# Optimization experiments

Measured on AMD Instinct MI355X. Metric: run time of the kernel, lower is better.

Reference implementation:

```python
import jax, jax.numpy as jnp
import numpy as np

N_ITERS = 10
OMEGA = 10
W_HALF = 512          # hpm.W
D = 2 * W_HALF        # real-lifted signal dim
BATCH = 4096
P_PREV = 8
EPS = 1e-8


def hard_thr(x, omega=OMEGA):
    # x: [B, D]; keep the omega largest-|x| entries per row, zero the rest
    # (equivalent to torch scatter-zero of the D-omega smallest |x|)
    _, idx = jax.lax.top_k(jnp.abs(x), omega)            # [B, omega]
    rows = jnp.arange(x.shape[0])[:, None]
    mask = jnp.zeros_like(x).at[rows, idx].set(1.0)
    return x * mask


def _spectral_density(z):
    # z: [B, D] -> squared complex magnitude summed over batch, min-max normalized
    w = z.shape[1] // 2
    p = z[:, :w] ** 2 + z[:, w:] ** 2                    # [B, W] (sign flip of imag part cancels)
    mD = p.sum(0)                                        # [W]
    return (mD - mD.min()) / (mD.max() - mD.min() + EPS)


def setup_inputs() -> dict:
    key = jax.random.key(0)
    k0, k1, k2 = jax.random.split(key, 3)
    x = jax.random.normal(k0, (BATCH, D), jnp.float32)
    prev_windows = jax.random.normal(k1, (P_PREV, BATCH, D), jnp.float32)
    # learned dictionary (stand-in for the real-lifted partial Fourier matrix)
    W_d = jax.random.normal(k2, (1, D, D), jnp.float32) / np.sqrt(D).astype(np.float32)
    L = jnp.float32(5.0)                                 # hpm.L (fixed Lipschitz constant)
    S = jnp.eye(D, dtype=jnp.float32)[None] - (1.0 / L) * jnp.matmul(
        jnp.swapaxes(W_d, 1, 2), W_d)                    # [1, D, D]
    lambda2 = jnp.float32(1.0)
    return {"x": x, "prev_windows": prev_windows, "W_d": W_d, "S": S,
            "lambda2": lambda2, "L": L}


def reference(x, prev_windows, W_d, S, lambda2, L):
    Wd0 = W_d[0]                                         # [D, D]
    S0 = S[0]                                            # [D, D]
    w = D // 2

    # B = (1/L * W_d) @ x   (column-vector matvec as row GEMM)
    b = (x @ Wd0.T) / L                                  # [B, D]

    # two warm-up ISTA/IHT steps
    z = hard_thr(b)
    c = b + z @ S0.T
    z = hard_thr(c)

    mD_normalized = _spectral_density(z)                 # [W]

    # ---- attention over previous windows (prev_windows non-empty branch) ----
    pw = prev_windows                                    # [P, B, D]
    p_prev = pw[:, :, :w] ** 2 + pw[:, :, w:] ** 2       # [P, B, W]
    mD_prev = p_prev.sum(1)                              # [P, W]
    mn = mD_prev.min(axis=1, keepdims=True)
    mx = mD_prev.max(axis=1, keepdims=True)
    prev_mDn = (mD_prev - mn) / (mx - mn + EPS)          # [P, W]

    att = prev_mDn @ mD_normalized[:, None]              # [P, 1]
    att = jax.nn.softmax(att / np.sqrt(float(w)).astype(np.float32), axis=0)
    pw_clamped = jnp.clip(pw, -150.0, 150.0)
    z = (pw_clamped * att[:, None]).sum(0) * lambda2     # [B, D]

    # ---- unrolled iterations ----
    for _ in range(N_ITERS):
        c = b + z @ S0.T
        z = hard_thr(c)

    mD_normalized = _spectral_density(z)                 # [W]
    return (mD_normalized, z)
```

## Files before the change

### kernel.cpp

```cpp
#include <hip/hip_runtime.h>
#include <stdint.h>

#define BATCH 4096
#define DIM   1024
#define PPREV 8

__device__ __forceinline__ int wave_max_i32(int v) {
    #pragma unroll
    for (int m = 1; m < 64; m <<= 1) v = max(v, __shfl_xor(v, m));
    return v;
}
__device__ __forceinline__ int wave_min_i32(int v) {
    #pragma unroll
    for (int m = 1; m < 64; m <<= 1) v = min(v, __shfl_xor(v, m));
    return v;
}
__device__ __forceinline__ int wave_sum_i32(int v) {
    #pragma unroll
    for (int m = 1; m < 64; m <<= 1) v += __shfl_xor(v, m);
    return v;
}
__device__ __forceinline__ int wave_exscan_i32(int v, int lane) {
    int s = v;
    #pragma unroll
    for (int off = 1; off < 64; off <<= 1) {
        int o = __shfl_up(s, off);
        s += (lane >= off) ? o : 0;
    }
    return s - v;
}


__device__ __forceinline__ int bound10_tbits(const int k[16], int lane) {
    int lm = k[0];
    #pragma unroll
    for (int s = 1; s < 16; ++s) lm = max(lm, k[s]);
    int cur = lm, tb = 0;
    #pragma unroll
    for (int r = 0; r < 10; ++r) {
        int m = wave_max_i32(cur);
        tb = m;
        unsigned long long ball = __ballot(cur == m);
        int wl = (int)__ffsll(ball) - 1;
        if (lane == wl) cur = 0;
    }
    return tb;
}

__device__ __forceinline__ void top10_full(const int kin[16], int sgn, int lane,
                                           int wi[10], float wv[10]) {
    int k[16];
    #pragma unroll
    for (int s = 0; s < 16; ++s) k[s] = kin[s];
    #pragma unroll
    for (int r = 0; r < 10; ++r) {
        int lm = k[0]; int ls = 0;
        #pragma unroll
        for (int s = 1; s < 16; ++s) { if (k[s] > lm) { lm = k[s]; ls = s; } }
        int m = wave_max_i32(lm);
        int cj = (lm == m) ? ((lane << 4) | ls) : 4096;
        int jw = wave_min_i32(cj);
        int wl = jw >> 4, ws = jw & 15;
        int sg = __shfl(sgn, wl);
        wi[r] = jw;
        wv[r] = __int_as_float(m | (((sg >> ws) & 1) << 31));
        if (lane == wl) {
            #pragma unroll
            for (int s = 0; s < 16; ++s) if (s == ws) k[s] = 0;
        }
    }
}

__device__ __forceinline__ bool top10_pruned(const float cz[16], const int k[16], int lane,
                                             float* svalw, int* sjw,
                                             int& tbits, int wi[10], float wv[10]) {
    int tb = tbits;
    int total;
    #pragma unroll 1
    for (int attempt = 0; ; ++attempt) {
        int c = 0;
        #pragma unroll
        for (int s = 0; s < 16; ++s) c += (k[s] >= tb) ? 1 : 0;
        total = wave_sum_i32(c);
        if (total >= 10) break;
        tb = (tb > 0x00800000) ? (tb - 0x00800000) : 0;
        if (attempt >= 20) tb = 0;
    }
    if (total > 64) return false;
    int cnt = 0;
    #pragma unroll
    for (int s = 0; s < 16; ++s) cnt += (k[s] >= tb) ? 1 : 0;
    int p = wave_exscan_i32(cnt, lane);
    #pragma unroll
    for (int s = 0; s < 16; ++s) {
        if (k[s] >= tb) { svalw[p] = cz[s]; sjw[p] = (lane << 4) | s; ++p; }
    }
    asm volatile("s_waitcnt lgkmcnt(0)" ::: "memory");
    float mv = 0.0f; int mj = 4096; int mk = 0;
    if (lane < total) { mv = svalw[lane]; mj = sjw[lane]; mk = __float_as_int(mv) & 0x7fffffff; }
    #pragma unroll
    for (int r = 0; r < 10; ++r) {
        int m = wave_max_i32(mk);
        int cj = (mk == m) ? mj : 4096;
        int jw = wave_min_i32(cj);
        unsigned long long ball = __ballot(mj == jw);
        int wl = (int)__ffsll(ball) - 1;
        wv[r] = __shfl(mv, wl);
        wi[r] = jw;
        mk = (mj == jw) ? 0 : mk;
    }
    tbits = __float_as_int(wv[9]) & 0x7fffffff;
    return true;
}

__device__ __forceinline__ void select10(const float cz[16], int lane,
                                         float* svalw, int* sjw,
                                         int& tbits, bool seeded,
                                         int wi[10], float wv[10]) {
    int k[16]; int sgn = 0;
    #pragma unroll
    for (int s = 0; s < 16; ++s) {
        int bb = __float_as_int(cz[s]);
        k[s] = bb & 0x7fffffff;
        sgn |= (int)(((unsigned)bb >> 31) << s);
    }
    if (!seeded) tbits = bound10_tbits(k, lane);
    if (!top10_pruned(cz, k, lane, svalw, sjw, tbits, wi, wv)) {
        top10_full(k, sgn, lane, wi, wv);
        tbits = __float_as_int(wv[9]) & 0x7fffffff;
    }
}

__device__ __forceinline__ void gather_ista(const float bz[16], float cz[16],
                                            const float* __restrict__ S,
                                            const int wi[10], const float wv[10], int lane) {
    #pragma unroll
    for (int s = 0; s < 16; ++s) cz[s] = bz[s];
    #pragma unroll
    for (int kk = 0; kk < 10; ++kk) {
        int row = __builtin_amdgcn_readfirstlane(wi[kk]);
        float wvs = __int_as_float(__builtin_amdgcn_readfirstlane(__float_as_int(wv[kk])));
        const float4* sp = (const float4*)(S + (size_t)row * DIM + (lane << 4));
        #pragma unroll
        for (int q = 0; q < 4; ++q) {
            float4 v = sp[q];
            cz[q*4+0] += wvs * v.x;
            cz[q*4+1] += wvs * v.y;
            cz[q*4+2] += wvs * v.z;
            cz[q*4+3] += wvs * v.w;
        }
    }
}

__global__ __launch_bounds__(256)
void warmup_rows(const float* __restrict__ b, const float* __restrict__ S,
                 int* __restrict__ sidx, float* __restrict__ sval) {
    __shared__ float s_v[4][64];
    __shared__ int   s_j[4][64];
    const int tid = threadIdx.x, lane = tid & 63, wid = tid >> 6;
    const int r = blockIdx.x * 4 + wid;
    const float* bp = b + (size_t)r * DIM + (lane << 4);
    float bz[16];
    #pragma unroll
    for (int q = 0; q < 4; ++q) {
        float4 v = ((const float4*)bp)[q];
        bz[q*4+0] = v.x; bz[q*4+1] = v.y; bz[q*4+2] = v.z; bz[q*4+3] = v.w;
    }
    int wi[10]; float wv[10]; int tbits = 0;
    select10(bz, lane, s_v[wid], s_j[wid], tbits, false, wi, wv);
    float cz[16];
    gather_ista(bz, cz, S, wi, wv, lane);
    select10(cz, lane, s_v[wid], s_j[wid], tbits, true, wi, wv);
    if (lane == 0) {
        #pragma unroll
        for (int kk = 0; kk < 10; ++kk) { sidx[r*10+kk] = wi[kk]; sval[r*10+kk] = wv[kk]; }
    }
}

__global__ __launch_bounds__(256)
void loop_rows(const float* __restrict__ c1, const float* __restrict__ b,
               const float* __restrict__ S, float* __restrict__ zout,
               int* __restrict__ sidx, float* __restrict__ sval) {
    __shared__ float s_v[4][64];
    __shared__ int   s_j[4][64];
    const int tid = threadIdx.x, lane = tid & 63, wid = tid >> 6;
    const int r = blockIdx.x * 4 + wid;
    const float* bp = b  + (size_t)r * DIM + (lane << 4);
    const float* cp = c1 + (size_t)r * DIM + (lane << 4);
    float bz[16], cz[16];
    #pragma unroll
    for (int q = 0; q < 4; ++q) {
        float4 v = ((const float4*)bp)[q];
        bz[q*4+0] = v.x; bz[q*4+1] = v.y; bz[q*4+2] = v.z; bz[q*4+3] = v.w;
        float4 u = ((const float4*)cp)[q];
        cz[q*4+0] = u.x; cz[q*4+1] = u.y; cz[q*4+2] = u.z; cz[q*4+3] = u.w;
    }
    int wi[10]; float wv[10]; int tbits = 0;
    select10(cz, lane, s_v[wid], s_j[wid], tbits, false, wi, wv);
    #pragma unroll 1
    for (int it = 0; it < 9; ++it) {
        gather_ista(bz, cz, S, wi, wv, lane);
        select10(cz, lane, s_v[wid], s_j[wid], tbits, true, wi, wv);
    }
    #pragma unroll
    for (int q = 0; q < 4; ++q) {
        float e[4];
        #pragma unroll
        for (int t = 0; t < 4; ++t) {
            int j = (lane << 4) | (q*4 + t);
            float v = 0.0f;
            #pragma unroll
            for (int kk = 0; kk < 10; ++kk) v = (wi[kk] == j) ? wv[kk] : v;
            e[t] = v;
        }
        float4 o; o.x = e[0]; o.y = e[1]; o.z = e[2]; o.w = e[3];
        ((float4*)(zout + (size_t)r * DIM + (lane << 4)))[q] = o;
    }
    if (lane == 0) {
        #pragma unroll
        for (int kk = 0; kk < 10; ++kk) { sidx[r*10+kk] = wi[kk]; sval[r*10+kk] = wv[kk]; }
    }
}

template<bool DIV_L, bool HAS_ADD>
__global__ __launch_bounds__(512)
void gemm128(const float* __restrict__ A, const float* __restrict__ B,
             const float* __restrict__ addM, float* __restrict__ C,
             const float* __restrict__ Lptr, int M, int N, int K) {
    __shared__ float As[16][132];
    __shared__ float Bs[16][132];
    const int tid = threadIdx.x;
    const int m0 = blockIdx.y * 128, n0 = blockIdx.x * 128;
    const int tx = tid & 15;
    const int ty = tid >> 4;
    const int srow = tid >> 2;
    const int sk   = (tid & 3) * 4;
    float acc[4][8] = {};
    const float* Ab = A + (size_t)(m0 + srow) * K + sk;
    const float* Bb = B + (size_t)(n0 + srow) * K + sk;
    for (int k0 = 0; k0 < K; k0 += 16) {
        float4 av = *(const float4*)(Ab + k0);
        float4 bv = *(const float4*)(Bb + k0);
        __syncthreads();
        As[sk+0][srow] = av.x; As[sk+1][srow] = av.y; As[sk+2][srow] = av.z; As[sk+3][srow] = av.w;
        Bs[sk+0][srow] = bv.x; Bs[sk+1][srow] = bv.y; Bs[sk+2][srow] = bv.z; Bs[sk+3][srow] = bv.w;
        __syncthreads();
        #pragma unroll
        for (int k = 0; k < 16; ++k) {
            float4 a4  = *(const float4*)&As[k][ty*4];
            float4 b40 = *(const float4*)&Bs[k][tx*8];
            float4 b41 = *(const float4*)&Bs[k][tx*8+4];
            float am[4] = {a4.x, a4.y, a4.z, a4.w};
            float bn[8] = {b40.x, b40.y, b40.z, b40.w, b41.x, b41.y, b41.z, b41.w};
            #pragma unroll
            for (int i = 0; i < 4; ++i)
                #pragma unroll
                for (int j = 0; j < 8; ++j)
                    acc[i][j] += am[i] * bn[j];
        }
    }
    const float invL = DIV_L ? (1.0f / *Lptr) : 1.0f;
    #pragma unroll
    for (int i = 0; i < 4; ++i) {
        size_t row = (size_t)(m0 + ty*4 + i);
        float* Cp = C + row * N + n0 + tx*8;
        #pragma unroll
        for (int j = 0; j < 8; ++j) {
            float r = acc[i][j];
            if (DIV_L) r *= invL;
            if (HAS_ADD) r += addM[row * N + n0 + tx*8 + j];
            Cp[j] = r;
        }
    }
}

__global__ void sparse_density_stage1(const int* __restrict__ sidx,
                                      const float* __restrict__ sval,
                                      float* __restrict__ partial) {
    const int w = threadIdx.x;
    const int blk = blockIdx.x;
    const int base = blk * 64 * 10;
    float acc = 0.0f;
    for (int e = 0; e < 640; ++e) {
        int d = sidx[base + e];
        float v = sval[base + e];
        if ((d & 511) == w) acc += v * v;
    }
    partial[blk * 512 + w] = acc;
}

__global__ void density_stage2(const float* __restrict__ partial, float* __restrict__ mD) {
    const int w = threadIdx.x;
    float acc = 0.0f;
    for (int i = 0; i < 64; ++i) acc += partial[i * 512 + w];
    mD[w] = acc;
}

__global__ void prev_density_stage1(const float* __restrict__ pw, float* __restrict__ partial) {
    const int p = blockIdx.x, chunk = blockIdx.y;
    const int w = threadIdx.x;
    const float* base = pw + ((size_t)p * BATCH + (size_t)chunk * 64) * DIM;
    float acc = 0.0f;
    for (int i = 0; i < 64; ++i) {
        float a = base[(size_t)i * DIM + w];
        float c = base[(size_t)i * DIM + 512 + w];
        acc += a * a + c * c;
    }
    partial[((size_t)(p * 64 + chunk)) * 512 + w] = acc;
}

__global__ void prev_density_stage2(const float* __restrict__ partial, float* __restrict__ mD_prev) {
    const int p = blockIdx.x; const int w = threadIdx.x;
    float acc = 0.0f;
    for (int i = 0; i < 64; ++i) acc += partial[((size_t)(p * 64 + i)) * 512 + w];
    mD_prev[p * 512 + w] = acc;
}

__device__ __forceinline__ float wave_fmax(float v) {
    #pragma unroll
    for (int m = 1; m < 64; m <<= 1) v = fmaxf(v, __shfl_xor(v, m));
    return v;
}
__device__ __forceinline__ float wave_fmin(float v) {
    #pragma unroll
    for (int m = 1; m < 64; m <<= 1) v = fminf(v, __shfl_xor(v, m));
    return v;
}
__device__ __forceinline__ float wave_fsum(float v) {
    #pragma unroll
    for (int m = 1; m < 64; m <<= 1) v += __shfl_xor(v, m);
    return v;
}

__global__ void attention_small(const float* __restrict__ mD1,
                                const float* __restrict__ mD_prev,
                                float* __restrict__ att) {
    __shared__ float att_l[PPREV];
    const int tid = threadIdx.x, lane = tid & 63, w = tid >> 6;
    float t8[8], u8[8];
    {
        const float4* m4 = (const float4*)(mD1 + lane * 8);
        float4 a = m4[0], bq = m4[1];
        t8[0]=a.x; t8[1]=a.y; t8[2]=a.z; t8[3]=a.w; t8[4]=bq.x; t8[5]=bq.y; t8[6]=bq.z; t8[7]=bq.w;
        const float4* p4 = (const float4*)(mD_prev + w * 512 + lane * 8);
        float4 c = p4[0], d = p4[1];
        u8[0]=c.x; u8[1]=c.y; u8[2]=c.z; u8[3]=c.w; u8[4]=d.x; u8[5]=d.y; u8[6]=d.z; u8[7]=d.w;
    }
    float mx = t8[0], mn = t8[0], pmx = u8[0], pmn = u8[0];
    #pragma unroll
    for (int i = 1; i < 8; ++i) {
        mx = fmaxf(mx, t8[i]); mn = fminf(mn, t8[i]);
        pmx = fmaxf(pmx, u8[i]); pmn = fminf(pmn, u8[i]);
    }
    mx = wave_fmax(mx); mn = wave_fmin(mn);
    pmx = wave_fmax(pmx); pmn = wave_fmin(pmn);
    const float inv  = 1.0f / (mx - mn + 1e-8f);
    const float pinv = 1.0f / (pmx - pmn + 1e-8f);
    float dot = 0.0f;
    #pragma unroll
    for (int i = 0; i < 8; ++i) dot += ((u8[i] - pmn) * pinv) * ((t8[i] - mn) * inv);
    dot = wave_fsum(dot);
    if (lane == 0) att_l[w] = dot / 22.627417f;
    __syncthreads();
    if (tid == 0) {
        float m = att_l[0];
        #pragma unroll
        for (int p = 1; p < PPREV; ++p) m = fmaxf(m, att_l[p]);
        float e[PPREV], s = 0.0f;
        #pragma unroll
        for (int p = 0; p < PPREV; ++p) { e[p] = expf(att_l[p] - m); s += e[p]; }
        #pragma unroll
        for (int p = 0; p < PPREV; ++p) att[p] = e[p] / s;
    }
}

__global__ __launch_bounds__(256)
void weighted_sum(const float* __restrict__ pw, const float* __restrict__ att,
                  const float* __restrict__ lam, float* __restrict__ zatt) {
    const size_t i = ((size_t)blockIdx.x * 256 + threadIdx.x) * 4;
    const float l2 = *lam;
    float a[PPREV];
    #pragma unroll
    for (int p = 0; p < PPREV; ++p) a[p] = att[p];
    float4 acc = make_float4(0.f, 0.f, 0.f, 0.f);
    #pragma unroll
    for (int p = 0; p < PPREV; ++p) {
        float4 v = *(const float4*)(pw + (size_t)p * BATCH * DIM + i);
        v.x = fminf(fmaxf(v.x, -150.f), 150.f);
        v.y = fminf(fmaxf(v.y, -150.f), 150.f);
        v.z = fminf(fmaxf(v.z, -150.f), 150.f);
        v.w = fminf(fmaxf(v.w, -150.f), 150.f);
        acc.x += v.x * a[p]; acc.y += v.y * a[p]; acc.z += v.z * a[p]; acc.w += v.w * a[p];
    }
    acc.x *= l2; acc.y *= l2; acc.z *= l2; acc.w *= l2;
    *(float4*)(zatt + i) = acc;
}

__global__ void finalize(const float* __restrict__ mD, float* __restrict__ out) {
    __shared__ float red[512];
    const int tid = threadIdx.x;
    float v = mD[tid];
    red[tid] = v; __syncthreads();
    for (int off = 256; off > 0; off >>= 1) { if (tid < off) red[tid] = fmaxf(red[tid], red[tid+off]); __syncthreads(); }
    float mx = red[0]; __syncthreads();
    red[tid] = v; __syncthreads();
    for (int off = 256; off > 0; off >>= 1) { if (tid < off) red[tid] = fminf(red[tid], red[tid+off]); __syncthreads(); }
    float mn = red[0];
    out[tid] = (v - mn) / (mx - mn + 1e-8f);
}

extern "C" void kernel_launch(void* const* d_in, const int* in_sizes, int n_in,
                              void* d_out, int out_size, void* d_ws, size_t ws_size,
                              hipStream_t stream) {
    const float* x   = (const float*)d_in[0];
    const float* pw  = (const float*)d_in[1];
    const float* Wd  = (const float*)d_in[2];
    const float* S   = (const float*)d_in[3];
    const float* lam = (const float*)d_in[4];
    const float* L   = (const float*)d_in[5];
    float* out = (float*)d_out;

    float* b       = (float*)d_ws;
    float* zatt    = b + (size_t)BATCH * DIM;
    float* pp_prev = zatt + (size_t)BATCH * DIM;
    float* pp_dens = pp_prev + 262144;
    float* mD1     = pp_dens + 32768;
    float* mD_prev = mD1 + 512;
    float* attw    = mD_prev + 4096;
    float* mD2     = attw + 8;
    float* sval1   = mD2 + 512;
    float* sval2   = sval1 + 40960;
    int*   sidx1   = (int*)(sval2 + 40960);
    int*   sidx2   = sidx1 + 40960;

    float* c1   = out + 512;
    float* zout = out + 512;

    const dim3 gg(DIM / 128, BATCH / 128);

    gemm128<true,  false><<<gg, 512, 0, stream>>>(x, Wd, nullptr, b, L, BATCH, DIM, DIM);
    warmup_rows<<<BATCH / 4, 256, 0, stream>>>(b, S, sidx1, sval1);
    sparse_density_stage1<<<64, 512, 0, stream>>>(sidx1, sval1, pp_dens);
    density_stage2<<<1, 512, 0, stream>>>(pp_dens, mD1);
    prev_density_stage1<<<dim3(PPREV, 64), 512, 0, stream>>>(pw, pp_prev);
    prev_density_stage2<<<PPREV, 512, 0, stream>>>(pp_prev, mD_prev);
    attention_small<<<1, 512, 0, stream>>>(mD1, mD_prev, attw);
    weighted_sum<<<(BATCH * DIM) / 1024, 256, 0, stream>>>(pw, attw, lam, zatt);
    gemm128<false, true ><<<gg, 512, 0, stream>>>(zatt, S, b, c1, nullptr, BATCH, DIM, DIM);
    loop_rows<<<BATCH / 4, 256, 0, stream>>>(c1, b, S, zout, sidx2, sval2);
    sparse_density_stage1<<<64, 512, 0, stream>>>(sidx2, sval2, pp_dens);
    density_stage2<<<1, 512, 0, stream>>>(pp_dens, mD2);
    finalize<<<1, 512, 0, stream>>>(mD2, out);
}
```

Baseline: 581.1 us.

## Bitonic top-10 selection, early exit on fixed point, one-wave blocks, fuse finalize

Replaces the serial max-reduction top-10 passes with wave-wide bitonic sorts, both for the seed threshold and for the candidate set. Candidates are compacted with ballot and mbcnt prefix counts. Adds an early break in the ISTA loop once the selected support and values repeat, which is exact because the iteration is deterministic. Blocks shrink to one wave per row, the gather uses per-lane indices instead of readfirstlane, and density_stage2 is fused into finalize.

```diff
diff --git a/kernel.cpp b/kernel.cpp
--- a/kernel.cpp
+++ b/kernel.cpp
@@ -15,37 +15,11 @@
     for (int m = 1; m < 64; m <<= 1) v = min(v, __shfl_xor(v, m));
     return v;
 }
-__device__ __forceinline__ int wave_sum_i32(int v) {
-    #pragma unroll
-    for (int m = 1; m < 64; m <<= 1) v += __shfl_xor(v, m);
-    return v;
-}
-__device__ __forceinline__ int wave_exscan_i32(int v, int lane) {
-    int s = v;
-    #pragma unroll
-    for (int off = 1; off < 64; off <<= 1) {
-        int o = __shfl_up(s, off);
-        s += (lane >= off) ? o : 0;
-    }
-    return s - v;
-}
-
-
-__device__ __forceinline__ int bound10_tbits(const int k[16], int lane) {
-    int lm = k[0];
-    #pragma unroll
-    for (int s = 1; s < 16; ++s) lm = max(lm, k[s]);
-    int cur = lm, tb = 0;
-    #pragma unroll
-    for (int r = 0; r < 10; ++r) {
-        int m = wave_max_i32(cur);
-        tb = m;
-        unsigned long long ball = __ballot(cur == m);
-        int wl = (int)__ffsll(ball) - 1;
-        if (lane == wl) cur = 0;
-    }
-    return tb;
-}
+__device__ __forceinline__ int lt_count(unsigned long long m) {
+    return __builtin_amdgcn_mbcnt_hi((unsigned)(m >> 32),
+           __builtin_amdgcn_mbcnt_lo((unsigned)m, 0));
+}
+
 
 __device__ __forceinline__ void top10_full(const int kin[16], int sgn, int lane,
                                            int wi[10], float wv[10]) {
@@ -71,52 +45,10 @@
     }
 }
 
-__device__ __forceinline__ bool top10_pruned(const float cz[16], const int k[16], int lane,
-                                             float* svalw, int* sjw,
-                                             int& tbits, int wi[10], float wv[10]) {
-    int tb = tbits;
-    int total;
-    #pragma unroll 1
-    for (int attempt = 0; ; ++attempt) {
-        int c = 0;
-        #pragma unroll
-        for (int s = 0; s < 16; ++s) c += (k[s] >= tb) ? 1 : 0;
-        total = wave_sum_i32(c);
-        if (total >= 10) break;
-        tb = (tb > 0x00800000) ? (tb - 0x00800000) : 0;
-        if (attempt >= 20) tb = 0;
-    }
-    if (total > 64) return false;
-    int cnt = 0;
-    #pragma unroll
-    for (int s = 0; s < 16; ++s) cnt += (k[s] >= tb) ? 1 : 0;
-    int p = wave_exscan_i32(cnt, lane);
-    #pragma unroll
-    for (int s = 0; s < 16; ++s) {
-        if (k[s] >= tb) { svalw[p] = cz[s]; sjw[p] = (lane << 4) | s; ++p; }
-    }
-    asm volatile("s_waitcnt lgkmcnt(0)" ::: "memory");
-    float mv = 0.0f; int mj = 4096; int mk = 0;
-    if (lane < total) { mv = svalw[lane]; mj = sjw[lane]; mk = __float_as_int(mv) & 0x7fffffff; }
-    #pragma unroll
-    for (int r = 0; r < 10; ++r) {
-        int m = wave_max_i32(mk);
-        int cj = (mk == m) ? mj : 4096;
-        int jw = wave_min_i32(cj);
-        unsigned long long ball = __ballot(mj == jw);
-        int wl = (int)__ffsll(ball) - 1;
-        wv[r] = __shfl(mv, wl);
-        wi[r] = jw;
-        mk = (mj == jw) ? 0 : mk;
-    }
-    tbits = __float_as_int(wv[9]) & 0x7fffffff;
-    return true;
-}
-
+template<bool SEEDED>
 __device__ __forceinline__ void select10(const float cz[16], int lane,
-                                         float* svalw, int* sjw,
-                                         int& tbits, bool seeded,
-                                         int wi[10], float wv[10]) {
+                                         int* s_kb, int* s_pay,
+                                         int& tbits, int wi[10], float wv[10]) {
     int k[16]; int sgn = 0;
     #pragma unroll
     for (int s = 0; s < 16; ++s) {
@@ -124,8 +56,70 @@
         k[s] = bb & 0x7fffffff;
         sgn |= (int)(((unsigned)bb >> 31) << s);
     }
-    if (!seeded) tbits = bound10_tbits(k, lane);
-    if (!top10_pruned(cz, k, lane, svalw, sjw, tbits, wi, wv)) {
+
+    if (!SEEDED) {
+        int lm = k[0];
+        #pragma unroll
+        for (int s = 1; s < 16; ++s) lm = max(lm, k[s]);
+        #pragma unroll
+        for (int k2 = 2; k2 <= 64; k2 <<= 1) {
+            #pragma unroll
+            for (int j = k2 >> 1; j > 0; j >>= 1) {
+                int p = __shfl_xor(lm, j);
+                bool keep_max = (((lane & k2) == 0) == ((lane & j) == 0));
+                if ((p > lm) == keep_max) lm = p;
+            }
+        }
+        tbits = __builtin_amdgcn_readlane(lm, 9);
+    }
+
+    int tb = tbits;
+    int total;
+    #pragma unroll 1
+    for (;;) {
+        total = 0;
+        #pragma unroll
+        for (int s = 0; s < 16; ++s)
+            total += __popcll(__ballot(k[s] >= tb));
+        if (total >= 10) break;
+        tb = (tb > 0x00800000) ? (tb - 0x00800000) : 0;
+    }
+
+    if (total <= 64) {
+        int base = 0;
+        #pragma unroll
+        for (int s = 0; s < 16; ++s) {
+            unsigned long long bs = __ballot(k[s] >= tb);
+            if (k[s] >= tb) {
+                int pos = base + lt_count(bs);
+                s_kb[pos]  = k[s];
+                s_pay[pos] = ((1023 - ((lane << 4) | s)) << 1) | ((sgn >> s) & 1);
+            }
+            base += __popcll(bs);
+        }
+        asm volatile("s_waitcnt lgkmcnt(0)" ::: "memory");
+        int kb = -1, pay = 0;
+        if (lane < total) { kb = s_kb[lane]; pay = s_pay[lane]; }
+        #pragma unroll
+        for (int k2 = 2; k2 <= 64; k2 <<= 1) {
+            #pragma unroll
+            for (int j = k2 >> 1; j > 0; j >>= 1) {
+                int pk = __shfl_xor(kb, j);
+                int pp = __shfl_xor(pay, j);
+                bool keep_max = (((lane & k2) == 0) == ((lane & j) == 0));
+                bool gt = (pk > kb) || ((pk == kb) && (pp > pay));
+                if (gt == keep_max) { kb = pk; pay = pp; }
+            }
+        }
+        #pragma unroll
+        for (int r = 0; r < 10; ++r) {
+            int kr = __builtin_amdgcn_readlane(kb, r);
+            int pr = __builtin_amdgcn_readlane(pay, r);
+            wi[r] = 1023 - (pr >> 1);
+            wv[r] = __int_as_float(kr | ((pr & 1) << 31));
+        }
+        tbits = __builtin_amdgcn_readlane(kb, 9);
+    } else {
         top10_full(k, sgn, lane, wi, wv);
         tbits = __float_as_int(wv[9]) & 0x7fffffff;
     }
@@ -138,9 +132,8 @@
     for (int s = 0; s < 16; ++s) cz[s] = bz[s];
     #pragma unroll
     for (int kk = 0; kk < 10; ++kk) {
-        int row = __builtin_amdgcn_readfirstlane(wi[kk]);
-        float wvs = __int_as_float(__builtin_amdgcn_readfirstlane(__float_as_int(wv[kk])));
-        const float4* sp = (const float4*)(S + (size_t)row * DIM + (lane << 4));
+        const float4* sp = (const float4*)(S + (size_t)wi[kk] * DIM + (lane << 4));
+        const float wvs = wv[kk];
         #pragma unroll
         for (int q = 0; q < 4; ++q) {
             float4 v = sp[q];
@@ -152,13 +145,13 @@
     }
 }
 
-__global__ __launch_bounds__(256)
+__global__ __launch_bounds__(64)
 void warmup_rows(const float* __restrict__ b, const float* __restrict__ S,
                  int* __restrict__ sidx, float* __restrict__ sval) {
-    __shared__ float s_v[4][64];
-    __shared__ int   s_j[4][64];
-    const int tid = threadIdx.x, lane = tid & 63, wid = tid >> 6;
-    const int r = blockIdx.x * 4 + wid;
+    __shared__ int s_kb[64];
+    __shared__ int s_pay[64];
+    const int lane = threadIdx.x;
+    const int r = blockIdx.x;
     const float* bp = b + (size_t)r * DIM + (lane << 4);
     float bz[16];
     #pragma unroll
@@ -167,24 +160,24 @@
         bz[q*4+0] = v.x; bz[q*4+1] = v.y; bz[q*4+2] = v.z; bz[q*4+3] = v.w;
     }
     int wi[10]; float wv[10]; int tbits = 0;
-    select10(bz, lane, s_v[wid], s_j[wid], tbits, false, wi, wv);
+    select10<false>(bz, lane, s_kb, s_pay, tbits, wi, wv);
     float cz[16];
     gather_ista(bz, cz, S, wi, wv, lane);
-    select10(cz, lane, s_v[wid], s_j[wid], tbits, true, wi, wv);
+    select10<true>(cz, lane, s_kb, s_pay, tbits, wi, wv);
     if (lane == 0) {
         #pragma unroll
         for (int kk = 0; kk < 10; ++kk) { sidx[r*10+kk] = wi[kk]; sval[r*10+kk] = wv[kk]; }
     }
 }
 
-__global__ __launch_bounds__(256)
+__global__ __launch_bounds__(64)
 void loop_rows(const float* __restrict__ c1, const float* __restrict__ b,
                const float* __restrict__ S, float* __restrict__ zout,
                int* __restrict__ sidx, float* __restrict__ sval) {
-    __shared__ float s_v[4][64];
-    __shared__ int   s_j[4][64];
-    const int tid = threadIdx.x, lane = tid & 63, wid = tid >> 6;
-    const int r = blockIdx.x * 4 + wid;
+    __shared__ int s_kb[64];
+    __shared__ int s_pay[64];
+    const int lane = threadIdx.x;
+    const int r = blockIdx.x;
     const float* bp = b  + (size_t)r * DIM + (lane << 4);
     const float* cp = c1 + (size_t)r * DIM + (lane << 4);
     float bz[16], cz[16];
@@ -196,11 +189,19 @@
         cz[q*4+0] = u.x; cz[q*4+1] = u.y; cz[q*4+2] = u.z; cz[q*4+3] = u.w;
     }
     int wi[10]; float wv[10]; int tbits = 0;
-    select10(cz, lane, s_v[wid], s_j[wid], tbits, false, wi, wv);
+    select10<false>(cz, lane, s_kb, s_pay, tbits, wi, wv);
+    int pwi[10], pwb[10];
     #pragma unroll 1
     for (int it = 0; it < 9; ++it) {
+        #pragma unroll
+        for (int kk = 0; kk < 10; ++kk) { pwi[kk] = wi[kk]; pwb[kk] = __float_as_int(wv[kk]); }
         gather_ista(bz, cz, S, wi, wv, lane);
-        select10(cz, lane, s_v[wid], s_j[wid], tbits, true, wi, wv);
+        select10<true>(cz, lane, s_kb, s_pay, tbits, wi, wv);
+        bool same = true;
+        #pragma unroll
+        for (int kk = 0; kk < 10; ++kk)
+            same = same && (wi[kk] == pwi[kk]) && (__float_as_int(wv[kk]) == pwb[kk]);
+        if (same) break;
     }
     #pragma unroll
     for (int q = 0; q < 4; ++q) {
@@ -396,10 +397,11 @@
     *(float4*)(zatt + i) = acc;
 }
 
-__global__ void finalize(const float* __restrict__ mD, float* __restrict__ out) {
+__global__ void finalize_fused(const float* __restrict__ partial, float* __restrict__ out) {
     __shared__ float red[512];
     const int tid = threadIdx.x;
-    float v = mD[tid];
+    float v = 0.0f;
+    for (int i = 0; i < 64; ++i) v += partial[i * 512 + tid];
     red[tid] = v; __syncthreads();
     for (int off = 256; off > 0; off >>= 1) { if (tid < off) red[tid] = fmaxf(red[tid], red[tid+off]); __syncthreads(); }
     float mx = red[0]; __syncthreads();
@@ -427,8 +429,7 @@
     float* mD1     = pp_dens + 32768;
     float* mD_prev = mD1 + 512;
     float* attw    = mD_prev + 4096;
-    float* mD2     = attw + 8;
-    float* sval1   = mD2 + 512;
+    float* sval1   = attw + 8;
     float* sval2   = sval1 + 40960;
     int*   sidx1   = (int*)(sval2 + 40960);
     int*   sidx2   = sidx1 + 40960;
@@ -439,7 +440,7 @@
     const dim3 gg(DIM / 128, BATCH / 128);
 
     gemm128<true,  false><<<gg, 512, 0, stream>>>(x, Wd, nullptr, b, L, BATCH, DIM, DIM);
-    warmup_rows<<<BATCH / 4, 256, 0, stream>>>(b, S, sidx1, sval1);
+    warmup_rows<<<BATCH, 64, 0, stream>>>(b, S, sidx1, sval1);
     sparse_density_stage1<<<64, 512, 0, stream>>>(sidx1, sval1, pp_dens);
     density_stage2<<<1, 512, 0, stream>>>(pp_dens, mD1);
     prev_density_stage1<<<dim3(PPREV, 64), 512, 0, stream>>>(pw, pp_prev);
@@ -447,8 +448,7 @@
     attention_small<<<1, 512, 0, stream>>>(mD1, mD_prev, attw);
     weighted_sum<<<(BATCH * DIM) / 1024, 256, 0, stream>>>(pw, attw, lam, zatt);
     gemm128<false, true ><<<gg, 512, 0, stream>>>(zatt, S, b, c1, nullptr, BATCH, DIM, DIM);
-    loop_rows<<<BATCH / 4, 256, 0, stream>>>(c1, b, S, zout, sidx2, sval2);
+    loop_rows<<<BATCH, 64, 0, stream>>>(c1, b, S, zout, sidx2, sval2);
     sparse_density_stage1<<<64, 512, 0, stream>>>(sidx2, sval2, pp_dens);
-    density_stage2<<<1, 512, 0, stream>>>(pp_dens, mD2);
-    finalize<<<1, 512, 0, stream>>>(mD2, out);
-}
+    finalize_fused<<<1, 512, 0, stream>>>(pp_dens, out);
+}
```

Result: slower. 596.8 us (+2.7%).
